# Kernel tuning notes

Hardware: AMD Instinct MI355X
Metric: run time of the kernel (lower is better)

Reference implementation:

```python
import jax, jax.numpy as jnp
import numpy as np

B, S, DM = 4, 2048, 512
H, D = 8, 64          # att_head, head_dim = att_dim // att_head
LEFT, RIGHT = 128, 128  # band_part(left_mask, right_mask)
LARGE = 1e30          # masked_softmax large number for fp32


def setup_inputs() -> dict:
    key = jax.random.key(0)
    ks = jax.random.split(key, 11)
    scale = 1.0 / np.sqrt(DM)
    x = jax.random.normal(ks[0], (B, S, DM), jnp.float32)
    Wq = jax.random.normal(ks[1], (DM, DM), jnp.float32) * scale
    bq = jnp.zeros((DM,), jnp.float32)
    Wk = jax.random.normal(ks[2], (DM, DM), jnp.float32) * scale
    bk = jnp.zeros((DM,), jnp.float32)
    Wv = jax.random.normal(ks[3], (DM, DM), jnp.float32) * scale
    bv = jnp.zeros((DM,), jnp.float32)
    Wo = jax.random.normal(ks[4], (DM, DM), jnp.float32) * scale
    bo = jnp.zeros((DM,), jnp.float32)
    x_len = jax.random.randint(ks[5], (B,), 0, 2048)
    return {"x": x, "Wq": Wq, "bq": bq, "Wk": Wk, "bk": bk,
            "Wv": Wv, "bv": bv, "Wo": Wo, "bo": bo, "x_len": x_len}


def reference(x, Wq, bq, Wk, bk, Wv, bv, Wo, bo, x_len):
    b, s, _ = x.shape
    # QKV projections, split into heads: [B,S,H,D]
    q = (x @ Wq + bq).reshape(b, s, H, D)
    k = (x @ Wk + bk).reshape(b, s, H, D)
    v = (x @ Wv + bv).reshape(b, s, H, D)
    # content energy: [B,H,Q,K], scaled by sqrt(head_dim)
    energy = jnp.einsum('bind,bjnd->bnij', q, k) / jnp.sqrt(jnp.float32(D))
    # banded mask (tf.linalg.band_part semantics): keep -LEFT <= j-i <= RIGHT
    i = jnp.arange(s)[:, None]
    j = jnp.arange(s)[None, :]
    band = ((j - i) <= RIGHT) & ((i - j) <= LEFT)            # [S,S]
    # key-length mask (tf.sequence_mask, expanded to [B,1,1,S])
    seq = jnp.arange(s)[None, :] < x_len[:, None]            # [B,S]
    mask = (band[None, None, :, :] & seq[:, None, None, :]).astype(energy.dtype)
    # masked softmax: energy - (1 - mask) * LARGE, softmax over keys
    att = jax.nn.softmax(energy - (1.0 - mask) * LARGE, axis=-1)
    # context: [B,Q,H,D] -> [B,S,H*D]
    ctx = jnp.einsum('bnij,bjnd->bind', att, v).reshape(b, s, H * D)
    # output projection (use_proj=True)
    return ctx @ Wo + bo
```

## Files before the change

### kernel.cpp

```cpp
#include <hip/hip_runtime.h>

#define S_LEN 2048
#define BATCH 4
#define DMODEL 512
#define NHEAD 8
#define HDIM 64
#define ROWS (BATCH * S_LEN)

using short8 = __attribute__((ext_vector_type(8))) short;
using f32x4  = __attribute__((ext_vector_type(4))) float;

__device__ __forceinline__ unsigned short f2bf(float f) {
  unsigned int u = __builtin_bit_cast(unsigned int, f);
  u += 0x7fffu + ((u >> 16) & 1u);
  return (unsigned short)(u >> 16);
}
__device__ __forceinline__ float bf2f(unsigned short h) {
  unsigned int u = ((unsigned int)h) << 16;
  return __builtin_bit_cast(float, u);
}
__device__ __forceinline__ void glds16(const void* g, void* l) {
  __builtin_amdgcn_global_load_lds((const __attribute__((address_space(1))) unsigned*)g,
                                   (__attribute__((address_space(3))) unsigned*)l, 16, 0, 0);
}

__global__ __launch_bounds__(256) void prep_kernel(const float* __restrict__ x,
                                                   const float* __restrict__ Wq,
                                                   const float* __restrict__ Wk,
                                                   const float* __restrict__ Wv,
                                                   const float* __restrict__ Wo,
                                                   unsigned short* __restrict__ xb,
                                                   unsigned short* __restrict__ WqkT,
                                                   unsigned short* __restrict__ WvT,
                                                   unsigned short* __restrict__ WoT) {
  __shared__ float t[32][33];
  const int blk = blockIdx.x, tid = threadIdx.x;
  if (blk < 2048) {
    const int base = (blk * 256 + tid) * 8;
    float4 f0 = *(const float4*)(x + base);
    float4 f1 = *(const float4*)(x + base + 4);
    uint4 o;
    o.x = (unsigned)f2bf(f0.x) | ((unsigned)f2bf(f0.y) << 16);
    o.y = (unsigned)f2bf(f0.z) | ((unsigned)f2bf(f0.w) << 16);
    o.z = (unsigned)f2bf(f1.x) | ((unsigned)f2bf(f1.y) << 16);
    o.w = (unsigned)f2bf(f1.z) | ((unsigned)f2bf(f1.w) << 16);
    *(uint4*)(xb + base) = o;
    return;
  }
  const int tb = blk - 2048;
  const int which = tb >> 8;
  const int tile = tb & 255;
  const float* W = which == 0 ? Wq : which == 1 ? Wk : which == 2 ? Wv : Wo;
  unsigned short* WT = which == 0 ? WqkT : which == 1 ? (WqkT + 512 * 512)
                      : which == 2 ? WvT : WoT;
  const int tx = tid & 31, ty = tid >> 5;
  const int x0 = (tile & 15) * 32, y0 = (tile >> 4) * 32;
#pragma unroll
  for (int r = 0; r < 4; r++)
    t[ty + 8 * r][tx] = W[(size_t)(y0 + ty + 8 * r) * DMODEL + x0 + tx];
  __syncthreads();
#pragma unroll
  for (int r = 0; r < 4; r++)
    WT[(size_t)(x0 + ty + 8 * r) * DMODEL + y0 + tx] = f2bf(t[tx][ty + 8 * r]);
}

__global__ __launch_bounds__(256, 2) void gemm_qkv_kernel(const unsigned short* __restrict__ xb,
                                                          const unsigned short* __restrict__ WqkT,
                                                          const unsigned short* __restrict__ WvT,
                                                          const float* __restrict__ bq,
                                                          const float* __restrict__ bk,
                                                          const float* __restrict__ bv,
                                                          const int* __restrict__ x_len,
                                                          unsigned short* __restrict__ Qb,
                                                          unsigned short* __restrict__ Kb,
                                                          unsigned short* __restrict__ Vt) {
  constexpr int K = DMODEL;
  __shared__ __align__(16) char smem[16384];
  char* As = smem;
  char* Bs = smem + 8192;
  const int bid = blockIdx.x;
  const bool vmode = bid < 256;
  const unsigned short *A, *Bt;
  int m0, n0;
  if (vmode) {
    m0 = (bid & 3) * 128;
    n0 = (bid >> 2) * 128;
    A = WvT; Bt = xb;
  } else {
    const int q = bid - 256;
    m0 = (q >> 3) * 128;
    n0 = (q & 7) * 128;
    A = xb; Bt = WqkT;
    const int xl = x_len[m0 >> 11];
    const int s0 = m0 & 2047;
    if (n0 >= DMODEL) { if (s0 >= xl) return; }
    else if (s0 >= xl + 128) return;
  }
  const int tid = threadIdx.x;
  const int wave = tid >> 6, lane = tid & 63;
  const int wr = wave >> 1, wc = wave & 1;
  const int lm = lane & 15, lq = lane >> 4;
  const int lr = lane >> 2;
  const int lc = (lane & 3) ^ ((lane >> 3) & 3);
  const unsigned short* gA0 = A + (size_t)(m0 + wave * 16 + lr) * K + lc * 8;
  const unsigned short* gA1 = A + (size_t)(m0 + (wave + 4) * 16 + lr) * K + lc * 8;
  const unsigned short* gB0 = Bt + (size_t)(n0 + wave * 16 + lr) * K + lc * 8;
  const unsigned short* gB1 = Bt + (size_t)(n0 + (wave + 4) * 16 + lr) * K + lc * 8;
  char* lA0 = As + wave * 1024 + lane * 16;
  char* lA1 = As + (wave + 4) * 1024 + lane * 16;
  char* lB0 = Bs + wave * 1024 + lane * 16;
  char* lB1 = Bs + (wave + 4) * 1024 + lane * 16;
  const int sw = (lm >> 1) & 3;
  int aoff[4], boff[4];
#pragma unroll
  for (int mi = 0; mi < 4; mi++)
    aoff[mi] = (wr * 64 + mi * 16 + lm) * 64 + (lq ^ sw) * 16;
#pragma unroll
  for (int ni = 0; ni < 4; ni++)
    boff[ni] = (wc * 64 + ni * 16 + lm) * 64 + (lq ^ sw) * 16;

  f32x4 acc[4][4] = {};
  for (int k0 = 0; k0 < K; k0 += 32) {
    __syncthreads();
    glds16(gA0 + k0, lA0);
    glds16(gA1 + k0, lA1);
    glds16(gB0 + k0, lB0);
    glds16(gB1 + k0, lB1);
    __syncthreads();
    short8 af[4], bfr[4];
#pragma unroll
    for (int mi = 0; mi < 4; mi++) af[mi] = *(const short8*)(As + aoff[mi]);
#pragma unroll
    for (int ni = 0; ni < 4; ni++) bfr[ni] = *(const short8*)(Bs + boff[ni]);
#pragma unroll
    for (int mi = 0; mi < 4; mi++)
#pragma unroll
      for (int ni = 0; ni < 4; ni++)
        acc[mi][ni] = __builtin_amdgcn_mfma_f32_16x16x32_bf16(af[mi], bfr[ni], acc[mi][ni], 0, 0, 0);
  }
#pragma unroll
  for (int mi = 0; mi < 4; mi++) {
    const int row0 = m0 + wr * 64 + mi * 16 + lq * 4;
#pragma unroll
    for (int ni = 0; ni < 4; ni++) {
      const int col = n0 + wc * 64 + ni * 16 + lm;
#pragma unroll
      for (int r = 0; r < 4; r++) {
        const int row = row0 + r;
        const float v = acc[mi][ni][r];
        if (vmode) {
          Vt[(size_t)row * ROWS + col] = f2bf(v + bv[row]);
        } else if (col < DMODEL) {
          Qb[(size_t)row * DMODEL + col] = f2bf(v + bq[col]);
        } else {
          Kb[(size_t)row * DMODEL + (col - DMODEL)] = f2bf(v + bk[col - DMODEL]);
        }
      }
    }
  }
}

__global__ __launch_bounds__(256) void vsum_kernel(const unsigned short* __restrict__ Vt,
                                                   float* __restrict__ vs) {
  const int wid = blockIdx.x * 4 + (threadIdx.x >> 6);
  const int lane = threadIdx.x & 63;
  const int b = wid >> 9, n = wid & 511;
  const unsigned short* row = Vt + (size_t)n * ROWS + b * S_LEN;
  float s = 0.f;
#pragma unroll
  for (int it = 0; it < 4; it++) {
    uint4 v = *(const uint4*)(row + it * 512 + lane * 8);
    unsigned int w[4] = {v.x, v.y, v.z, v.w};
#pragma unroll
    for (int e = 0; e < 4; e++) {
      s += bf2f((unsigned short)(w[e] & 0xffffu));
      s += bf2f((unsigned short)(w[e] >> 16));
    }
  }
#pragma unroll
  for (int off = 1; off < 64; off <<= 1) s += __shfl_xor(s, off, 64);
  if (lane == 0) vs[(size_t)b * DMODEL + n] = s;
}

__global__ __launch_bounds__(256) void tailrow_kernel(const float* __restrict__ vsum,
                                                      const unsigned short* __restrict__ WoT,
                                                      const float* __restrict__ bo,
                                                      float* __restrict__ trow) {
  const int b = blockIdx.y;
  const int wave = threadIdx.x >> 6, lane = threadIdx.x & 63;
  const float* vs = vsum + b * DMODEL + lane * 8;
  float vreg[8];
  *(float4*)vreg = *(const float4*)vs;
  *(float4*)(vreg + 4) = *(const float4*)(vs + 4);
#pragma unroll
  for (int ci = 0; ci < 8; ci++) {
    const int c = blockIdx.x * 32 + wave * 8 + ci;
    const uint4 wv = *(const uint4*)(WoT + (size_t)c * DMODEL + lane * 8);
    const unsigned int w[4] = {wv.x, wv.y, wv.z, wv.w};
    float acc = 0.f;
#pragma unroll
    for (int e = 0; e < 4; e++) {
      acc += vreg[2 * e] * bf2f((unsigned short)(w[e] & 0xffffu));
      acc += vreg[2 * e + 1] * bf2f((unsigned short)(w[e] >> 16));
    }
#pragma unroll
    for (int off = 1; off < 64; off <<= 1) acc += __shfl_xor(acc, off, 64);
    if (lane == 0) trow[b * DMODEL + c] = bo[c] + acc * (1.f / 2048.f);
  }
}

__global__ __launch_bounds__(256) void attn_kernel(const unsigned short* __restrict__ Q,
                                                   const unsigned short* __restrict__ K,
                                                   const unsigned short* __restrict__ Vt,
                                                   const int* __restrict__ x_len,
                                                   const float* __restrict__ vsum,
                                                   unsigned short* __restrict__ ctx) {
  __shared__ unsigned short Ks[32][72];
  __shared__ unsigned short Vs[64][40];
  __shared__ unsigned short Ps[4][16][40];
  const int tid = threadIdx.x;
  const int wave = tid >> 6, lane = tid & 63;
  const int lm = lane & 15, lq = lane >> 4;
  const int b = blockIdx.z, h = blockIdx.y;
  const int i0 = blockIdx.x * 64;
  const int q0 = i0 + wave * 16;
  const int xlen = x_len[b];
  const int t0 = min(S_LEN, xlen + 128);
  if ((i0 & ~127) >= t0) return;

  const size_t qoff = (size_t)(b * S_LEN + q0 + lm) * DMODEL + h * HDIM + lq * 8;
  const short8 aq0 = *(const short8*)(Q + qoff);
  const short8 aq1 = *(const short8*)(Q + qoff + 32);

  const int krow = tid >> 3, kchk = (tid & 7) * 8;
  const int vdim = tid >> 2, vchk = (tid & 3) * 8;

  f32x4 oacc[4] = {};
  float lrow[4] = {0.f, 0.f, 0.f, 0.f};

  for (int kt = 0; kt < 10; kt++) {
    const int jt0 = i0 - 128 + kt * 32;
    if (jt0 + 31 < 0 || jt0 >= xlen) continue;
    __syncthreads();
    {
      const int jr = jt0 + krow;
      const int jrc = min(max(jr, 0), S_LEN - 1);
      *(uint4*)&Ks[krow][kchk] =
          *(const uint4*)(K + (size_t)(b * S_LEN + jrc) * DMODEL + h * HDIM + kchk);
      const int jv = jt0 + vchk;
      const int jvc = min(max(jv, 0), S_LEN - 8);
      *(uint4*)&Vs[vdim][vchk] =
          *(const uint4*)(Vt + (size_t)(h * HDIM + vdim) * ROWS + b * S_LEN + jvc);
    }
    __syncthreads();
    if (jt0 + 31 < q0 - 128 || jt0 > q0 + 143) continue;

    f32x4 sv[2];
#pragma unroll
    for (int sub = 0; sub < 2; sub++) {
      const short8 bk0 = *(const short8*)&Ks[sub * 16 + lm][lq * 8];
      const short8 bk1 = *(const short8*)&Ks[sub * 16 + lm][32 + lq * 8];
      f32x4 s = {};
      s = __builtin_amdgcn_mfma_f32_16x16x32_bf16(aq0, bk0, s, 0, 0, 0);
      s = __builtin_amdgcn_mfma_f32_16x16x32_bf16(aq1, bk1, s, 0, 0, 0);
      sv[sub] = s;
    }
    float p[2][4];
#pragma unroll
    for (int sub = 0; sub < 2; sub++) {
      const int j = jt0 + sub * 16 + lm;
      const bool jv = (j >= 0) && (j < xlen);
#pragma unroll
      for (int r = 0; r < 4; r++) {
        const int i = q0 + lq * 4 + r;
        const bool ok = jv && (j - i <= 128) && (i - j <= 128);
        const float pv = ok ? __expf(sv[sub][r] * 0.125f) : 0.f;
        p[sub][r] = pv;
        lrow[r] += pv;
      }
    }
#pragma unroll
    for (int r = 0; r < 4; r++) {
      Ps[wave][lq * 4 + r][lm] = f2bf(p[0][r]);
      Ps[wave][lq * 4 + r][16 + lm] = f2bf(p[1][r]);
    }
    const short8 pf = *(const short8*)&Ps[wave][lm][lq * 8];
#pragma unroll
    for (int dt = 0; dt < 4; dt++) {
      const short8 bv = *(const short8*)&Vs[dt * 16 + lm][lq * 8];
      oacc[dt] = __builtin_amdgcn_mfma_f32_16x16x32_bf16(pf, bv, oacc[dt], 0, 0, 0);
    }
  }
#pragma unroll
  for (int r = 0; r < 4; r++)
#pragma unroll
    for (int off = 1; off < 16; off <<= 1) lrow[r] += __shfl_xor(lrow[r], off, 64);

#pragma unroll
  for (int r = 0; r < 4; r++) {
    const int i = q0 + lq * 4 + r;
    const size_t obase = (size_t)(b * S_LEN + i) * DMODEL + h * HDIM;
    if (lrow[r] > 0.f) {
      const float inv = 1.f / lrow[r];
#pragma unroll
      for (int dt = 0; dt < 4; dt++)
        ctx[obase + dt * 16 + lm] = f2bf(oacc[dt][r] * inv);
    } else {
#pragma unroll
      for (int dt = 0; dt < 4; dt++)
        ctx[obase + dt * 16 + lm] =
            f2bf(vsum[(size_t)b * DMODEL + h * HDIM + dt * 16 + lm] * (1.f / 2048.f));
    }
  }
}

__global__ __launch_bounds__(256, 2) void gemm_out_kernel(const unsigned short* __restrict__ A,
                                                          const unsigned short* __restrict__ Bt,
                                                          const float* __restrict__ bias,
                                                          const int* __restrict__ x_len,
                                                          const float* __restrict__ trow,
                                                          float* __restrict__ out) {
  constexpr int K = DMODEL;
  __shared__ __align__(16) char smem[16384];
  char* As = smem;
  char* Bs = smem + 8192;
  const int tid = threadIdx.x;
  const int m0 = blockIdx.y * 128, n0 = blockIdx.x * 128;
  {
    const int xl = x_len[m0 >> 11];
    if ((m0 & 2047) >= min(S_LEN, xl + 128)) {
      const float4 val = *(const float4*)(trow + (m0 >> 11) * DMODEL + n0 + (tid & 31) * 4);
      float* obase = out + (size_t)m0 * DMODEL + n0 + (tid & 31) * 4;
#pragma unroll
      for (int r = tid >> 5; r < 128; r += 8)
        *(float4*)(obase + (size_t)r * DMODEL) = val;
      return;
    }
  }
  const int wave = tid >> 6, lane = tid & 63;
  const int wr = wave >> 1, wc = wave & 1;
  const int lm = lane & 15, lq = lane >> 4;
  const int lr = lane >> 2;
  const int lc = (lane & 3) ^ ((lane >> 3) & 3);
  const unsigned short* gA0 = A + (size_t)(m0 + wave * 16 + lr) * K + lc * 8;
  const unsigned short* gA1 = A + (size_t)(m0 + (wave + 4) * 16 + lr) * K + lc * 8;
  const unsigned short* gB0 = Bt + (size_t)(n0 + wave * 16 + lr) * K + lc * 8;
  const unsigned short* gB1 = Bt + (size_t)(n0 + (wave + 4) * 16 + lr) * K + lc * 8;
  char* lA0 = As + wave * 1024 + lane * 16;
  char* lA1 = As + (wave + 4) * 1024 + lane * 16;
  char* lB0 = Bs + wave * 1024 + lane * 16;
  char* lB1 = Bs + (wave + 4) * 1024 + lane * 16;
  const int sw = (lm >> 1) & 3;
  int aoff[4], boff[4];
#pragma unroll
  for (int mi = 0; mi < 4; mi++)
    aoff[mi] = (wr * 64 + mi * 16 + lm) * 64 + (lq ^ sw) * 16;
#pragma unroll
  for (int ni = 0; ni < 4; ni++)
    boff[ni] = (wc * 64 + ni * 16 + lm) * 64 + (lq ^ sw) * 16;

  f32x4 acc[4][4] = {};
  for (int k0 = 0; k0 < K; k0 += 32) {
    __syncthreads();
    glds16(gA0 + k0, lA0);
    glds16(gA1 + k0, lA1);
    glds16(gB0 + k0, lB0);
    glds16(gB1 + k0, lB1);
    __syncthreads();
    short8 af[4], bfr[4];
#pragma unroll
    for (int mi = 0; mi < 4; mi++) af[mi] = *(const short8*)(As + aoff[mi]);
#pragma unroll
    for (int ni = 0; ni < 4; ni++) bfr[ni] = *(const short8*)(Bs + boff[ni]);
#pragma unroll
    for (int mi = 0; mi < 4; mi++)
#pragma unroll
      for (int ni = 0; ni < 4; ni++)
        acc[mi][ni] = __builtin_amdgcn_mfma_f32_16x16x32_bf16(af[mi], bfr[ni], acc[mi][ni], 0, 0, 0);
  }
#pragma unroll
  for (int mi = 0; mi < 4; mi++) {
    const int row0 = m0 + wr * 64 + mi * 16 + lq * 4;
#pragma unroll
    for (int ni = 0; ni < 4; ni++) {
      const int col = n0 + wc * 64 + ni * 16 + lm;
#pragma unroll
      for (int r = 0; r < 4; r++)
        out[(size_t)(row0 + r) * DMODEL + col] = acc[mi][ni][r] + bias[col];
    }
  }
}

extern "C" void kernel_launch(void* const* d_in, const int* in_sizes, int n_in,
                              void* d_out, int out_size, void* d_ws, size_t ws_size,
                              hipStream_t stream) {
  (void)in_sizes; (void)n_in; (void)out_size; (void)ws_size;
  const float* x  = (const float*)d_in[0];
  const float* Wq = (const float*)d_in[1];
  const float* bq = (const float*)d_in[2];
  const float* Wk = (const float*)d_in[3];
  const float* bk = (const float*)d_in[4];
  const float* Wv = (const float*)d_in[5];
  const float* bv = (const float*)d_in[6];
  const float* Wo = (const float*)d_in[7];
  const float* bo = (const float*)d_in[8];
  const int* x_len = (const int*)d_in[9];

  char* ws = (char*)d_ws;
  const size_t MB = 1024 * 1024;
  unsigned short* xb   = (unsigned short*)(ws + 0 * MB);
  unsigned short* Qb   = (unsigned short*)(ws + 8 * MB);
  unsigned short* Kb   = (unsigned short*)(ws + 16 * MB);
  unsigned short* Vt   = (unsigned short*)(ws + 24 * MB);
  unsigned short* Cx   = (unsigned short*)(ws + 32 * MB);
  unsigned short* WqkT = (unsigned short*)(ws + 40 * MB);
  unsigned short* WvT  = (unsigned short*)(ws + 41 * MB);
  unsigned short* WoT  = (unsigned short*)(ws + 41 * MB + 512 * 1024);
  float* vsum          = (float*)(ws + 42 * MB);
  float* trow          = (float*)(ws + 42 * MB + 8192);

  prep_kernel<<<3072, 256, 0, stream>>>(x, Wq, Wk, Wv, Wo, xb, WqkT, WvT, WoT);
  gemm_qkv_kernel<<<768, 256, 0, stream>>>(xb, WqkT, WvT, bq, bk, bv, x_len, Qb, Kb, Vt);
  vsum_kernel<<<512, 256, 0, stream>>>(Vt, vsum);
  tailrow_kernel<<<dim3(16, 4), 256, 0, stream>>>(vsum, WoT, bo, trow);
  attn_kernel<<<dim3(32, 8, 4), 256, 0, stream>>>(Qb, Kb, Vt, x_len, vsum, Cx);
  gemm_out_kernel<<<dim3(4, 64), 256, 0, stream>>>(Cx, WoT, bo, x_len, trow, (float*)d_out);
}
```

Measured before the change: 148.9 us.

## Compute V column sums algebraically from x sums and fold tail kernels into neighbors

The separate vsum and tailrow kernels are removed. V's per-batch column sum is now computed as (sum of x rows)·Wv + S·bv: prep_kernel gets extra blocks that produce partial row sums of x in fp32, and qkv_kernel gets extra blocks that finish the projection. The tail-row projection through Wo is folded into extra blocks of attn_kernel. This cuts the launch count from six to four and avoids re-reading the full V tensor, at the cost of strided fp32 column reads of x and sums that differ slightly from summing the bf16-rounded V.

```diff
diff --git a/kernel.cpp b/kernel.cpp
--- a/kernel.cpp
+++ b/kernel.cpp
@@ -32,7 +32,8 @@
                                                    unsigned short* __restrict__ xb,
                                                    unsigned short* __restrict__ WqkT,
                                                    unsigned short* __restrict__ WvT,
-                                                   unsigned short* __restrict__ WoT) {
+                                                   unsigned short* __restrict__ WoT,
+                                                   float* __restrict__ xpart) {
   __shared__ float t[32][33];
   const int blk = blockIdx.x, tid = threadIdx.x;
   if (blk < 2048) {
@@ -47,38 +48,77 @@
     *(uint4*)(xb + base) = o;
     return;
   }
-  const int tb = blk - 2048;
-  const int which = tb >> 8;
-  const int tile = tb & 255;
-  const float* W = which == 0 ? Wq : which == 1 ? Wk : which == 2 ? Wv : Wo;
-  unsigned short* WT = which == 0 ? WqkT : which == 1 ? (WqkT + 512 * 512)
-                      : which == 2 ? WvT : WoT;
-  const int tx = tid & 31, ty = tid >> 5;
-  const int x0 = (tile & 15) * 32, y0 = (tile >> 4) * 32;
-#pragma unroll
-  for (int r = 0; r < 4; r++)
-    t[ty + 8 * r][tx] = W[(size_t)(y0 + ty + 8 * r) * DMODEL + x0 + tx];
-  __syncthreads();
-#pragma unroll
-  for (int r = 0; r < 4; r++)
-    WT[(size_t)(x0 + ty + 8 * r) * DMODEL + y0 + tx] = f2bf(t[tx][ty + 8 * r]);
-}
-
-__global__ __launch_bounds__(256, 2) void gemm_qkv_kernel(const unsigned short* __restrict__ xb,
-                                                          const unsigned short* __restrict__ WqkT,
-                                                          const unsigned short* __restrict__ WvT,
-                                                          const float* __restrict__ bq,
-                                                          const float* __restrict__ bk,
-                                                          const float* __restrict__ bv,
-                                                          const int* __restrict__ x_len,
-                                                          unsigned short* __restrict__ Qb,
-                                                          unsigned short* __restrict__ Kb,
-                                                          unsigned short* __restrict__ Vt) {
-  constexpr int K = DMODEL;
+  if (blk < 3072) {
+    const int tb = blk - 2048;
+    const int which = tb >> 8, tile = tb & 255;
+    const float* W = which == 0 ? Wq : which == 1 ? Wk : which == 2 ? Wv : Wo;
+    unsigned short* WT = which == 0 ? WqkT : which == 1 ? (WqkT + 512 * 512)
+                        : which == 2 ? WvT : WoT;
+    const int tx = tid & 31, ty = tid >> 5;
+    const int x0 = (tile & 15) * 32, y0 = (tile >> 4) * 32;
+#pragma unroll
+    for (int r = 0; r < 4; r++)
+      t[ty + 8 * r][tx] = W[(size_t)(y0 + ty + 8 * r) * DMODEL + x0 + tx];
+    __syncthreads();
+#pragma unroll
+    for (int r = 0; r < 4; r++)
+      WT[(size_t)(x0 + ty + 8 * r) * DMODEL + y0 + tx] = f2bf(t[tx][ty + 8 * r]);
+    return;
+  }
+  const int u = blk - 3072;
+  const int b = u >> 4, cg = (u >> 3) & 1, rc = u & 7;
+  const float* base = x + (size_t)(b * S_LEN + rc * 256) * DMODEL + cg * 256 + tid;
+  float s = 0.f;
+  for (int j = 0; j < 256; j++) s += base[(size_t)j * DMODEL];
+  xpart[u * 256 + tid] = s;
+}
+
+__global__ __launch_bounds__(256, 2) void qkv_kernel(const unsigned short* __restrict__ xb,
+                                                     const unsigned short* __restrict__ WqkT,
+                                                     const unsigned short* __restrict__ WvT,
+                                                     const float* __restrict__ bq,
+                                                     const float* __restrict__ bk,
+                                                     const float* __restrict__ bv,
+                                                     const int* __restrict__ x_len,
+                                                     const float* __restrict__ xpart,
+                                                     unsigned short* __restrict__ Qb,
+                                                     unsigned short* __restrict__ Kb,
+                                                     unsigned short* __restrict__ Vt,
+                                                     float* __restrict__ vsum) {
   __shared__ __align__(16) char smem[16384];
-  char* As = smem;
-  char* Bs = smem + 8192;
   const int bid = blockIdx.x;
+  const int tid = threadIdx.x;
+  if (bid >= 768) {
+    const int u = bid - 768;
+    const int b = u >> 5;
+    const int wave = tid >> 6, lane = tid & 63;
+    const int cg = lane >> 5, ko = (lane & 31) * 8;
+    float xs[8] = {};
+#pragma unroll
+    for (int rc = 0; rc < 8; rc++) {
+      const float* p = xpart + ((b * 16 + cg * 8 + rc) << 8) + ko;
+      float4 a0 = *(const float4*)p;
+      float4 a1 = *(const float4*)(p + 4);
+      xs[0] += a0.x; xs[1] += a0.y; xs[2] += a0.z; xs[3] += a0.w;
+      xs[4] += a1.x; xs[5] += a1.y; xs[6] += a1.z; xs[7] += a1.w;
+    }
+#pragma unroll
+    for (int ci = 0; ci < 4; ci++) {
+      const int f = (u & 31) * 16 + wave * 4 + ci;
+      const uint4 wv = *(const uint4*)(WvT + (size_t)f * DMODEL + lane * 8);
+      const unsigned int w[4] = {wv.x, wv.y, wv.z, wv.w};
+      float acc = 0.f;
+#pragma unroll
+      for (int e = 0; e < 4; e++) {
+        acc += xs[2 * e] * bf2f((unsigned short)(w[e] & 0xffffu));
+        acc += xs[2 * e + 1] * bf2f((unsigned short)(w[e] >> 16));
+      }
+#pragma unroll
+      for (int off = 1; off < 64; off <<= 1) acc += __shfl_xor(acc, off, 64);
+      if (lane == 0) vsum[b * DMODEL + f] = acc + 2048.f * bv[f];
+    }
+    return;
+  }
   const bool vmode = bid < 256;
   const unsigned short *A, *Bt;
   int m0, n0;
@@ -96,16 +136,17 @@
     if (n0 >= DMODEL) { if (s0 >= xl) return; }
     else if (s0 >= xl + 128) return;
   }
-  const int tid = threadIdx.x;
+  char* As = smem;
+  char* Bs = smem + 8192;
   const int wave = tid >> 6, lane = tid & 63;
   const int wr = wave >> 1, wc = wave & 1;
   const int lm = lane & 15, lq = lane >> 4;
   const int lr = lane >> 2;
   const int lc = (lane & 3) ^ ((lane >> 3) & 3);
-  const unsigned short* gA0 = A + (size_t)(m0 + wave * 16 + lr) * K + lc * 8;
-  const unsigned short* gA1 = A + (size_t)(m0 + (wave + 4) * 16 + lr) * K + lc * 8;
-  const unsigned short* gB0 = Bt + (size_t)(n0 + wave * 16 + lr) * K + lc * 8;
-  const unsigned short* gB1 = Bt + (size_t)(n0 + (wave + 4) * 16 + lr) * K + lc * 8;
+  const unsigned short* gA0 = A + (size_t)(m0 + wave * 16 + lr) * DMODEL + lc * 8;
+  const unsigned short* gA1 = A + (size_t)(m0 + (wave + 4) * 16 + lr) * DMODEL + lc * 8;
+  const unsigned short* gB0 = Bt + (size_t)(n0 + wave * 16 + lr) * DMODEL + lc * 8;
+  const unsigned short* gB1 = Bt + (size_t)(n0 + (wave + 4) * 16 + lr) * DMODEL + lc * 8;
   char* lA0 = As + wave * 1024 + lane * 16;
   char* lA1 = As + (wave + 4) * 1024 + lane * 16;
   char* lB0 = Bs + wave * 1024 + lane * 16;
@@ -113,14 +154,11 @@
   const int sw = (lm >> 1) & 3;
   int aoff[4], boff[4];
 #pragma unroll
-  for (int mi = 0; mi < 4; mi++)
-    aoff[mi] = (wr * 64 + mi * 16 + lm) * 64 + (lq ^ sw) * 16;
-#pragma unroll
-  for (int ni = 0; ni < 4; ni++)
-    boff[ni] = (wc * 64 + ni * 16 + lm) * 64 + (lq ^ sw) * 16;
-
+  for (int mi = 0; mi < 4; mi++) aoff[mi] = (wr * 64 + mi * 16 + lm) * 64 + (lq ^ sw) * 16;
+#pragma unroll
+  for (int ni = 0; ni < 4; ni++) boff[ni] = (wc * 64 + ni * 16 + lm) * 64 + (lq ^ sw) * 16;
   f32x4 acc[4][4] = {};
-  for (int k0 = 0; k0 < K; k0 += 32) {
+  for (int k0 = 0; k0 < DMODEL; k0 += 32) {
     __syncthreads();
     glds16(gA0 + k0, lA0);
     glds16(gA1 + k0, lA1);
@@ -160,84 +198,59 @@
   }
 }
 
-__global__ __launch_bounds__(256) void vsum_kernel(const unsigned short* __restrict__ Vt,
-                                                   float* __restrict__ vs) {
-  const int wid = blockIdx.x * 4 + (threadIdx.x >> 6);
-  const int lane = threadIdx.x & 63;
-  const int b = wid >> 9, n = wid & 511;
-  const unsigned short* row = Vt + (size_t)n * ROWS + b * S_LEN;
-  float s = 0.f;
-#pragma unroll
-  for (int it = 0; it < 4; it++) {
-    uint4 v = *(const uint4*)(row + it * 512 + lane * 8);
-    unsigned int w[4] = {v.x, v.y, v.z, v.w};
-#pragma unroll
-    for (int e = 0; e < 4; e++) {
-      s += bf2f((unsigned short)(w[e] & 0xffffu));
-      s += bf2f((unsigned short)(w[e] >> 16));
-    }
-  }
-#pragma unroll
-  for (int off = 1; off < 64; off <<= 1) s += __shfl_xor(s, off, 64);
-  if (lane == 0) vs[(size_t)b * DMODEL + n] = s;
-}
-
-__global__ __launch_bounds__(256) void tailrow_kernel(const float* __restrict__ vsum,
-                                                      const unsigned short* __restrict__ WoT,
-                                                      const float* __restrict__ bo,
-                                                      float* __restrict__ trow) {
-  const int b = blockIdx.y;
-  const int wave = threadIdx.x >> 6, lane = threadIdx.x & 63;
-  const float* vs = vsum + b * DMODEL + lane * 8;
-  float vreg[8];
-  *(float4*)vreg = *(const float4*)vs;
-  *(float4*)(vreg + 4) = *(const float4*)(vs + 4);
-#pragma unroll
-  for (int ci = 0; ci < 8; ci++) {
-    const int c = blockIdx.x * 32 + wave * 8 + ci;
-    const uint4 wv = *(const uint4*)(WoT + (size_t)c * DMODEL + lane * 8);
-    const unsigned int w[4] = {wv.x, wv.y, wv.z, wv.w};
-    float acc = 0.f;
-#pragma unroll
-    for (int e = 0; e < 4; e++) {
-      acc += vreg[2 * e] * bf2f((unsigned short)(w[e] & 0xffffu));
-      acc += vreg[2 * e + 1] * bf2f((unsigned short)(w[e] >> 16));
-    }
-#pragma unroll
-    for (int off = 1; off < 64; off <<= 1) acc += __shfl_xor(acc, off, 64);
-    if (lane == 0) trow[b * DMODEL + c] = bo[c] + acc * (1.f / 2048.f);
-  }
-}
-
 __global__ __launch_bounds__(256) void attn_kernel(const unsigned short* __restrict__ Q,
                                                    const unsigned short* __restrict__ K,
                                                    const unsigned short* __restrict__ Vt,
                                                    const int* __restrict__ x_len,
                                                    const float* __restrict__ vsum,
+                                                   const unsigned short* __restrict__ WoT,
+                                                   const float* __restrict__ bo,
+                                                   float* __restrict__ trow,
                                                    unsigned short* __restrict__ ctx) {
   __shared__ unsigned short Ks[32][72];
   __shared__ unsigned short Vs[64][40];
   __shared__ unsigned short Ps[4][16][40];
   const int tid = threadIdx.x;
+  const int unit = blockIdx.x;
   const int wave = tid >> 6, lane = tid & 63;
-  const int lm = lane & 15, lq = lane >> 4;
-  const int b = blockIdx.z, h = blockIdx.y;
-  const int i0 = blockIdx.x * 64;
-  const int q0 = i0 + wave * 16;
+  if (unit >= 1024) {
+    const int u = unit - 1024;
+    const int b = u >> 4;
+    const float* vs = vsum + b * DMODEL + lane * 8;
+    float vreg[8];
+    *(float4*)vreg = *(const float4*)vs;
+    *(float4*)(vreg + 4) = *(const float4*)(vs + 4);
+#pragma unroll
+    for (int ci = 0; ci < 8; ci++) {
+      const int c = (u & 15) * 32 + wave * 8 + ci;
+      const uint4 wv = *(const uint4*)(WoT + (size_t)c * DMODEL + lane * 8);
+      const unsigned int w[4] = {wv.x, wv.y, wv.z, wv.w};
+      float acc = 0.f;
+#pragma unroll
+      for (int e = 0; e < 4; e++) {
+        acc += vreg[2 * e] * bf2f((unsigned short)(w[e] & 0xffffu));
+        acc += vreg[2 * e + 1] * bf2f((unsigned short)(w[e] >> 16));
+      }
+#pragma unroll
+      for (int off = 1; off < 64; off <<= 1) acc += __shfl_xor(acc, off, 64);
+      if (lane == 0) trow[b * DMODEL + c] = bo[c] + acc * (1.f / 2048.f);
+    }
+    return;
+  }
+  const int b = unit >> 8, h = (unit >> 5) & 7;
+  const int i0 = (unit & 31) * 64;
   const int xlen = x_len[b];
   const int t0 = min(S_LEN, xlen + 128);
   if ((i0 & ~127) >= t0) return;
-
+  const int lm = lane & 15, lq = lane >> 4;
+  const int q0 = i0 + wave * 16;
   const size_t qoff = (size_t)(b * S_LEN + q0 + lm) * DMODEL + h * HDIM + lq * 8;
   const short8 aq0 = *(const short8*)(Q + qoff);
   const short8 aq1 = *(const short8*)(Q + qoff + 32);
-
   const int krow = tid >> 3, kchk = (tid & 7) * 8;
   const int vdim = tid >> 2, vchk = (tid & 3) * 8;
-
   f32x4 oacc[4] = {};
   float lrow[4] = {0.f, 0.f, 0.f, 0.f};
-
   for (int kt = 0; kt < 10; kt++) {
     const int jt0 = i0 - 128 + kt * 32;
     if (jt0 + 31 < 0 || jt0 >= xlen) continue;
@@ -254,7 +267,6 @@
     }
     __syncthreads();
     if (jt0 + 31 < q0 - 128 || jt0 > q0 + 143) continue;
-
     f32x4 sv[2];
 #pragma unroll
     for (int sub = 0; sub < 2; sub++) {
@@ -295,7 +307,6 @@
   for (int r = 0; r < 4; r++)
 #pragma unroll
     for (int off = 1; off < 16; off <<= 1) lrow[r] += __shfl_xor(lrow[r], off, 64);
-
 #pragma unroll
   for (int r = 0; r < 4; r++) {
     const int i = q0 + lq * 4 + r;
@@ -314,38 +325,35 @@
   }
 }
 
-__global__ __launch_bounds__(256, 2) void gemm_out_kernel(const unsigned short* __restrict__ A,
-                                                          const unsigned short* __restrict__ Bt,
-                                                          const float* __restrict__ bias,
-                                                          const int* __restrict__ x_len,
-                                                          const float* __restrict__ trow,
-                                                          float* __restrict__ out) {
-  constexpr int K = DMODEL;
+__global__ __launch_bounds__(256, 2) void out_kernel(const unsigned short* __restrict__ A,
+                                                     const unsigned short* __restrict__ Bt,
+                                                     const float* __restrict__ bias,
+                                                     const int* __restrict__ x_len,
+                                                     const float* __restrict__ trow,
+                                                     float* __restrict__ out) {
   __shared__ __align__(16) char smem[16384];
+  const int tid = threadIdx.x;
+  const int m0 = (blockIdx.x >> 2) * 128, n0 = (blockIdx.x & 3) * 128;
+  const int xl = x_len[m0 >> 11];
+  if ((m0 & 2047) >= min(S_LEN, xl + 128)) {
+    const float4 val = *(const float4*)(trow + (m0 >> 11) * DMODEL + n0 + (tid & 31) * 4);
+    float* obase = out + (size_t)m0 * DMODEL + n0 + (tid & 31) * 4;
+#pragma unroll
+    for (int r = tid >> 5; r < 128; r += 8)
+      *(float4*)(obase + (size_t)r * DMODEL) = val;
+    return;
+  }
   char* As = smem;
   char* Bs = smem + 8192;
-  const int tid = threadIdx.x;
-  const int m0 = blockIdx.y * 128, n0 = blockIdx.x * 128;
-  {
-    const int xl = x_len[m0 >> 11];
-    if ((m0 & 2047) >= min(S_LEN, xl + 128)) {
-      const float4 val = *(const float4*)(trow + (m0 >> 11) * DMODEL + n0 + (tid & 31) * 4);
-      float* obase = out + (size_t)m0 * DMODEL + n0 + (tid & 31) * 4;
-#pragma unroll
-      for (int r = tid >> 5; r < 128; r += 8)
-        *(float4*)(obase + (size_t)r * DMODEL) = val;
-      return;
-    }
-  }
   const int wave = tid >> 6, lane = tid & 63;
   const int wr = wave >> 1, wc = wave & 1;
   const int lm = lane & 15, lq = lane >> 4;
   const int lr = lane >> 2;
   const int lc = (lane & 3) ^ ((lane >> 3) & 3);
-  const unsigned short* gA0 = A + (size_t)(m0 + wave * 16 + lr) * K + lc * 8;
-  const unsigned short* gA1 = A + (size_t)(m0 + (wave + 4) * 16 + lr) * K + lc * 8;
-  const unsigned short* gB0 = Bt + (size_t)(n0 + wave * 16 + lr) * K + lc * 8;
-  const unsigned short* gB1 = Bt + (size_t)(n0 + (wave + 4) * 16 + lr) * K + lc * 8;
+  const unsigned short* gA0 = A + (size_t)(m0 + wave * 16 + lr) * DMODEL + lc * 8;
+  const unsigned short* gA1 = A + (size_t)(m0 + (wave + 4) * 16 + lr) * DMODEL + lc * 8;
+  const unsigned short* gB0 = Bt + (size_t)(n0 + wave * 16 + lr) * DMODEL + lc * 8;
+  const unsigned short* gB1 = Bt + (size_t)(n0 + (wave + 4) * 16 + lr) * DMODEL + lc * 8;
   char* lA0 = As + wave * 1024 + lane * 16;
   char* lA1 = As + (wave + 4) * 1024 + lane * 16;
   char* lB0 = Bs + wave * 1024 + lane * 16;
@@ -353,14 +361,11 @@
   const int sw = (lm >> 1) & 3;
   int aoff[4], boff[4];
 #pragma unroll
-  for (int mi = 0; mi < 4; mi++)
-    aoff[mi] = (wr * 64 + mi * 16 + lm) * 64 + (lq ^ sw) * 16;
-#pragma unroll
-  for (int ni = 0; ni < 4; ni++)
-    boff[ni] = (wc * 64 + ni * 16 + lm) * 64 + (lq ^ sw) * 16;
-
+  for (int mi = 0; mi < 4; mi++) aoff[mi] = (wr * 64 + mi * 16 + lm) * 64 + (lq ^ sw) * 16;
+#pragma unroll
+  for (int ni = 0; ni < 4; ni++) boff[ni] = (wc * 64 + ni * 16 + lm) * 64 + (lq ^ sw) * 16;
   f32x4 acc[4][4] = {};
-  for (int k0 = 0; k0 < K; k0 += 32) {
+  for (int k0 = 0; k0 < DMODEL; k0 += 32) {
     __syncthreads();
     glds16(gA0 + k0, lA0);
     glds16(gA1 + k0, lA1);
@@ -418,11 +423,11 @@
   unsigned short* WoT  = (unsigned short*)(ws + 41 * MB + 512 * 1024);
   float* vsum          = (float*)(ws + 42 * MB);
   float* trow          = (float*)(ws + 42 * MB + 8192);
-
-  prep_kernel<<<3072, 256, 0, stream>>>(x, Wq, Wk, Wv, Wo, xb, WqkT, WvT, WoT);
-  gemm_qkv_kernel<<<768, 256, 0, stream>>>(xb, WqkT, WvT, bq, bk, bv, x_len, Qb, Kb, Vt);
-  vsum_kernel<<<512, 256, 0, stream>>>(Vt, vsum);
-  tailrow_kernel<<<dim3(16, 4), 256, 0, stream>>>(vsum, WoT, bo, trow);
-  attn_kernel<<<dim3(32, 8, 4), 256, 0, stream>>>(Qb, Kb, Vt, x_len, vsum, Cx);
-  gemm_out_kernel<<<dim3(4, 64), 256, 0, stream>>>(Cx, WoT, bo, x_len, trow, (float*)d_out);
-}
+  float* xpart         = (float*)(ws + 43 * MB);
+
+  prep_kernel<<<3136, 256, 0, stream>>>(x, Wq, Wk, Wv, Wo, xb, WqkT, WvT, WoT, xpart);
+  qkv_kernel<<<896, 256, 0, stream>>>(xb, WqkT, WvT, bq, bk, bv, x_len, xpart,
+                                      Qb, Kb, Vt, vsum);
+  attn_kernel<<<1088, 256, 0, stream>>>(Qb, Kb, Vt, x_len, vsum, WoT, bo, trow, Cx);
+  out_kernel<<<256, 256, 0, stream>>>(Cx, WoT, bo, x_len, trow, (float*)d_out);
+}
```

New measurement: 150.1 us. No clear change (+0.8%).
